# Performance work log

Measured on AMD Instinct MI355X. Metric: run time of the kernel, lower is better.

## Reference

```python
import jax, jax.numpy as jnp
import numpy as np


def _conv(x, w, b=None):
    # x: [B,C,H,W], w: [O,I,kh,kw], 'same' padding for odd kernels
    pad_h = (w.shape[2] - 1) // 2
    pad_w = (w.shape[3] - 1) // 2
    y = jax.lax.conv_general_dilated(
        x, w, window_strides=(1, 1),
        padding=[(pad_h, pad_h), (pad_w, pad_w)],
        dimension_numbers=("NCHW", "OIHW", "NCHW"))
    if b is not None:
        y = y + b[None, :, None, None]
    return y


def setup_inputs() -> dict:
    key = jax.random.key(0)
    ks = jax.random.split(key, 14)
    B, L_I, L_H, MAZE, F, OUT = 32, 8, 128, 64, 5, 16
    s = 0.05  # weight scale
    return {
        "X": jax.random.normal(ks[0], (B, L_I, MAZE, MAZE), jnp.float32),
        "hid_w": jax.random.normal(ks[1], (L_H, L_I, 3, 3), jnp.float32) * s,
        "hid_b": jax.random.normal(ks[2], (L_H,), jnp.float32) * s,
        "h0_w": jax.random.normal(ks[3], (L_H, L_H, 3, 3), jnp.float32) * s,
        "h0_b": jax.random.normal(ks[4], (L_H,), jnp.float32) * s,
        "c0_w": jax.random.normal(ks[5], (L_H, L_H, 3, 3), jnp.float32) * s,
        "c0_b": jax.random.normal(ks[6], (L_H,), jnp.float32) * s,
        "conv_w": jax.random.normal(ks[7], (1, L_H, F, F), jnp.float32) * s,
        "conv_b": jax.random.normal(ks[8], (1,), jnp.float32) * s,
        "W_ih": jax.random.normal(ks[9], (4 * L_H, 1), jnp.float32) * s,
        "W_hh": jax.random.normal(ks[10], (4 * L_H, L_H), jnp.float32) * s,
        "b_ih": jnp.zeros((4 * L_H,), jnp.float32),
        "b_hh": jnp.zeros((4 * L_H,), jnp.float32),
        "policy_w": jax.random.normal(ks[11], (OUT, L_H, 1, 1), jnp.float32) * s,
        "k": 10,
    }


def reference(X, hid_w, hid_b, h0_w, h0_b, c0_w, c0_b, conv_w, conv_b,
              W_ih, W_hh, b_ih, b_hh, policy_w, k):
    # hid: [B, l_h, H, W]
    hid = _conv(X, hid_w, hid_b)
    # torch .transpose(1,3).view(-1,l_h): keep as [B, W, H, l_h]
    h = jnp.transpose(_conv(hid, h0_w, h0_b), (0, 3, 2, 1))
    c = jnp.transpose(_conv(hid, c0_w, c0_b), (0, 3, 2, 1))
    bias = b_ih + b_hh

    def step(carry, _):
        h, c = carry
        h_map = jnp.transpose(h, (0, 3, 2, 1))          # [B, l_h, H, W]
        inp = jnp.transpose(_conv(h_map, conv_w, conv_b), (0, 3, 2, 1))  # [B,W,H,1]
        # PyTorch LSTMCell gate order: i, f, g, o
        gates = inp @ W_ih.T + h @ W_hh.T + bias        # [B, W, H, 4*l_h]
        i, f, g, o = jnp.split(gates, 4, axis=-1)
        c_new = jax.nn.sigmoid(f) * c + jax.nn.sigmoid(i) * jnp.tanh(g)
        h_new = jax.nn.sigmoid(o) * jnp.tanh(c_new)
        return (h_new, c_new), None

    (h, c), _ = jax.lax.scan(step, (h, c), None, length=k - 1)
    hk = jnp.transpose(h, (0, 3, 2, 1))                 # [B, l_h, H, W]
    logits = _conv(hk, policy_w, None)                  # 1x1 conv, no bias
    return logits
```

## Files before the change

kernel.cpp:

```cpp
#include <hip/hip_runtime.h>
#include <math.h>


typedef _Float16 f16;
typedef _Float16 f16x8 __attribute__((ext_vector_type(8)));
typedef float    f32x4 __attribute__((ext_vector_type(4)));

#define NB 32
#define HWD 64
#define NPIX (NB*HWD*HWD)

#define OB_HID   ((size_t)0)
#define OB_CC    ((size_t)33554432)
#define OB_HA    ((size_t)100663296)
#define OB_HB    ((size_t)134217728)
#define OB_DA    ((size_t)167772160)
#define OB_DB    ((size_t)176160768)
#define OB_WCB   ((size_t)184549376)
#define OB_WGB   ((size_t)185139200)
#define OB_WIB   ((size_t)185270272)
#define OB_W5B   ((size_t)185303040)
#define OB_BS2   ((size_t)185311232)
#define WS_BYTES ((size_t)185313280)

__device__ __forceinline__ float sigm(float x){ return 1.f/(1.f+__expf(-x)); }
__device__ __forceinline__ float tanhx(float x){ return 1.f - 2.f/(1.f+__expf(2.f*x)); }

__global__ void kTrans(const float* __restrict__ h0w, const float* __restrict__ c0w,
                       const float* __restrict__ whh, const float* __restrict__ cw5,
                       const float* __restrict__ wih, const float* __restrict__ bih,
                       const float* __restrict__ bhh, const float* __restrict__ cb,
                       f16* __restrict__ wcb, f16* __restrict__ wgb,
                       f16* __restrict__ wib, f16* __restrict__ w5b,
                       float* __restrict__ bs2)
{
    int e = blockIdx.x*256 + threadIdx.x;
    if (e < 294912) {
        int j = e & 7, l = (e >> 3) & 63, kk = (e >> 9) & 3;
        int nt = (e >> 11) & 15, tap = e >> 15;
        int c = (nt & 7)*16 + (l & 15);
        int k = kk*32 + (l >> 4)*8 + j;
        const float* src = (nt < 8) ? h0w : c0w;
        wcb[e] = (f16)src[((size_t)c*128 + k)*9 + tap];
    }
    if (e < 65536) {
        int j = e & 7, l = (e >> 3) & 63, fb = e >> 9;
        int nt = fb >> 2, kk = fb & 3;
        int cg = nt*16 + (l & 15), k = kk*32 + (l >> 4)*8 + j;
        wgb[e] = (f16)whh[(size_t)cg*128 + k];
    }
    if (e < 16384) {
        int l = (e >> 3) & 63, nt = e >> 9;
        wib[e] = (f16)wih[nt*16 + (l & 15)];
    }
    if (e < 4096) {
        int j = e & 7, l = (e >> 3) & 63, fb = e >> 9;
        int nt = fb >> 2, kk = fb & 3;
        int n = nt*16 + (l & 15), k = kk*32 + (l >> 4)*8 + j;
        w5b[e] = (n < 25) ? (f16)cw5[k*25 + n] : (f16)0.f;
    }
    if (e < 512) bs2[e] = bih[e] + bhh[e] + cb[0]*wih[e];
}

__global__ __launch_bounds__(256) void kHid(const float* __restrict__ X,
                                            const float* __restrict__ hw,
                                            const float* __restrict__ hb,
                                            f16* __restrict__ hid)
{
    __shared__ float Ws[128*73];
    __shared__ float Xs[6*6*8];
    int t = threadIdx.x;
    int blk = blockIdx.x;
    int b = blk >> 8, ti = (blk >> 4) & 15, tj = blk & 15;
    int i0 = ti*4, j0 = tj*4;
    for (int e = t; e < 9216; e += 256) {
        int c = e/72, q = e - c*72;
        Ws[c*73 + q] = hw[e];
    }
    for (int e = t; e < 288; e += 256) {
        int pos = e >> 3, ci = e & 7;
        int gi = i0 + pos/6 - 1, gj = j0 + pos%6 - 1;
        float v = 0.f;
        if ((unsigned)gi < 64u && (unsigned)gj < 64u)
            v = X[(((size_t)b*8 + ci)*64 + gi)*64 + gj];
        Xs[pos*8 + ci] = v;
    }
    __syncthreads();
    int c = t & 127, ph = t >> 7;
    float bv = hb[c];
    for (int p = ph*8; p < ph*8 + 8; ++p) {
        int pi = p >> 2, pj = p & 3;
        float acc = bv;
        #pragma unroll
        for (int ci = 0; ci < 8; ++ci)
            #pragma unroll
            for (int dy = 0; dy < 3; ++dy)
                #pragma unroll
                for (int dx = 0; dx < 3; ++dx)
                    acc += Xs[((pi+dy)*6 + (pj+dx))*8 + ci] * Ws[c*73 + ci*9 + dy*3 + dx];
        hid[(((size_t)b*64 + i0+pi)*64 + (j0+pj))*128 + c] = (f16)acc;
    }
}

__global__ __launch_bounds__(256,2) void kInit(const f16* __restrict__ hid,
                                               const f16* __restrict__ wcb,
                                               const f16* __restrict__ w5b,
                                               const float* __restrict__ h0b,
                                               const float* __restrict__ c0b,
                                               f16* __restrict__ h0out,
                                               float* __restrict__ cc,
                                               f16* __restrict__ dout)
{
    __shared__ f16 sHalo[100*128];
    int t = threadIdx.x;
    int blk = blockIdx.x;
    int b = blk >> 6, ti = (blk >> 3) & 7, tj = blk & 7;
    int i0 = ti*8, j0 = tj*8;
    int l = t & 63, wn = t >> 6;

    for (int e = t; e < 1600; e += 256) {
        int pos = e >> 4, ch = e & 15;
        int gi = i0 + pos/10 - 1, gj = j0 + pos%10 - 1;
        f16x8 v = {0,0,0,0,0,0,0,0};
        if ((unsigned)gi < 64u && (unsigned)gj < 64u)
            v = *(const f16x8*)(hid + ((((size_t)b*64 + gi)*64 + gj)*128) + ch*8);
        *(f16x8*)&sHalo[(pos*16 + (ch ^ (pos & 7)))*8] = v;
    }
    __syncthreads();

    f32x4 acc[4][4];
    #pragma unroll
    for (int mi = 0; mi < 4; ++mi)
        #pragma unroll
        for (int q = 0; q < 4; ++q) acc[mi][q] = (f32x4){0.f,0.f,0.f,0.f};

    for (int tap = 0; tap < 9; ++tap) {
        int dy = tap/3, dx = tap - dy*3;
        f16x8 a[4][4];
        #pragma unroll
        for (int mi = 0; mi < 4; ++mi) {
            int mrow = mi*16 + (l & 15);
            int pos = ((mrow >> 3) + dy)*10 + (mrow & 7) + dx;
            #pragma unroll
            for (int kk = 0; kk < 4; ++kk)
                a[mi][kk] = *(const f16x8*)&sHalo[(pos*16 + ((kk*4 + (l >> 4)) ^ (pos & 7)))*8];
        }
        #pragma unroll
        for (int q = 0; q < 4; ++q) {
            int nt = wn*4 + q;
            f16x8 bf[4];
            #pragma unroll
            for (int kk = 0; kk < 4; ++kk)
                bf[kk] = *(const f16x8*)(wcb + ((size_t)((tap*16 + nt)*4 + kk)*64 + l)*8);
            #pragma unroll
            for (int mi = 0; mi < 4; ++mi)
                #pragma unroll
                for (int kk = 0; kk < 4; ++kk)
                    acc[mi][q] = __builtin_amdgcn_mfma_f32_16x16x32_f16(a[mi][kk], bf[kk], acc[mi][q], 0, 0, 0);
        }
    }

    __syncthreads();
    f16* sH = sHalo;

    int cl = l & 15;
    bool isC = (wn >= 2);
    #pragma unroll
    for (int q = 0; q < 4; ++q) {
        int c = ((wn & 1)*4 + q)*16 + cl;
        float bv = isC ? c0b[c] : h0b[c];
        #pragma unroll
        for (int mi = 0; mi < 4; ++mi) {
            int mbase = mi*16 + (l >> 4)*4;
            if (isC) {
                float4 cv;
                cv.x = acc[mi][q][0] + bv; cv.y = acc[mi][q][1] + bv;
                cv.z = acc[mi][q][2] + bv; cv.w = acc[mi][q][3] + bv;
                *(float4*)(cc + (size_t)blk*8192 + (size_t)c*64 + mbase) = cv;
            } else {
                #pragma unroll
                for (int r = 0; r < 4; ++r) {
                    int m = mbase + r;
                    size_t gp = ((((size_t)b*64 + i0 + (m >> 3))*64 + j0 + (m & 7))*128) + c;
                    f16 hv = (f16)(acc[mi][q][r] + bv);
                    h0out[gp] = hv;
                    sH[(m*16 + ((c >> 3) ^ (m & 7)))*8 + (c & 7)] = hv;
                }
            }
        }
    }
    __syncthreads();

    {
        int m0 = wn*16 + (l & 15);
        f16x8 av[4];
        #pragma unroll
        for (int kk = 0; kk < 4; ++kk)
            av[kk] = *(const f16x8*)&sH[(m0*16 + ((kk*4 + (l >> 4)) ^ (m0 & 7)))*8];
        #pragma unroll
        for (int nt = 0; nt < 2; ++nt) {
            f32x4 dc = {0.f,0.f,0.f,0.f};
            #pragma unroll
            for (int kk = 0; kk < 4; ++kk)
                dc = __builtin_amdgcn_mfma_f32_16x16x32_f16(av[kk],
                        *(const f16x8*)(w5b + ((size_t)((nt*4 + kk)*64 + l))*8), dc, 0, 0, 0);
            #pragma unroll
            for (int r = 0; r < 4; ++r) {
                int mm = wn*16 + (l >> 4)*4 + r;
                size_t gp = ((((size_t)b*64 + i0 + (mm >> 3))*64 + j0 + (mm & 7))*32) + nt*16 + (l & 15);
                dout[gp] = (f16)dc[r];
            }
        }
    }
}

__global__ __launch_bounds__(256,4) void kFuse(const f16* __restrict__ hin,
                                               const f16* __restrict__ din,
                                               const f16* __restrict__ wgb,
                                               const f16* __restrict__ wib,
                                               const f16* __restrict__ w5b,
                                               const float* __restrict__ bs2,
                                               float* __restrict__ cc,
                                               f16* __restrict__ hout,
                                               f16* __restrict__ dout)
{
    __shared__ f16 sDH[144*32];
    __shared__ f16 sH[64*128];
    int t = threadIdx.x;
    int blk = blockIdx.x;
    int b = blk >> 6, ti = (blk >> 3) & 7, tj = blk & 7;
    int i0 = ti*8, j0 = tj*8;
    int l = t & 63, w = t >> 6;
    int wn = w >> 1, wm = w & 1;
    int cl = l & 15;

    f16x8 a[2][4];
    #pragma unroll
    for (int mi = 0; mi < 2; ++mi) {
        int m = (wm + mi*2)*16 + (l & 15);
        size_t gp = (((size_t)b*64 + i0 + (m >> 3))*64 + j0 + (m & 7))*128;
        #pragma unroll
        for (int kk = 0; kk < 4; ++kk)
            a[mi][kk] = *(const f16x8*)(hin + gp + kk*32 + (l >> 4)*8);
    }
    for (int e = t; e < 576; e += 256) {
        int pos = e >> 2, ch = e & 3;
        int gi = i0 + pos/12 - 2, gj = j0 + pos%12 - 2;
        f16x8 v = {0,0,0,0,0,0,0,0};
        if ((unsigned)gi < 64u && (unsigned)gj < 64u)
            v = *(const f16x8*)(din + (((size_t)b*64 + gi)*64 + gj)*32 + ch*8);
        *(f16x8*)&sDH[pos*32 + ch*8] = v;
    }
    __syncthreads();

    f16x8 adh[2];
    #pragma unroll
    for (int mi = 0; mi < 2; ++mi) {
        int m = (wm + mi*2)*16 + (l & 15);
        int pi = m >> 3, pj = m & 7;
        f16 tmp[8];
        #pragma unroll
        for (int j = 0; j < 8; ++j) {
            int kp = (l >> 4)*8 + j;
            int kpc = (kp < 25) ? kp : 0;
            int ty = kpc/5, tx = kpc - ty*5;
            f16 v = sDH[((pi + ty)*12 + (pj + tx))*32 + kpc];
            tmp[j] = (kp < 25) ? v : (f16)0.f;
        }
        adh[mi] = *(f16x8*)tmp;
    }

    bool doD = (dout != nullptr);
    #pragma unroll
    for (int q = 0; q < 4; ++q) {
        f32x4 acc2[2][4];
        #pragma unroll
        for (int mi = 0; mi < 2; ++mi)
            #pragma unroll
            for (int g = 0; g < 4; ++g) acc2[mi][g] = (f32x4){0.f,0.f,0.f,0.f};
        #pragma unroll
        for (int g = 0; g < 4; ++g) {
            int nt = g*8 + wn*4 + q;
            #pragma unroll
            for (int kk = 0; kk < 4; ++kk) {
                f16x8 bf = *(const f16x8*)(wgb + ((size_t)((nt*4 + kk)*64 + l))*8);
                #pragma unroll
                for (int mi = 0; mi < 2; ++mi)
                    acc2[mi][g] = __builtin_amdgcn_mfma_f32_16x16x32_f16(a[mi][kk], bf, acc2[mi][g], 0, 0, 0);
            }
            f16x8 be = *(const f16x8*)(wib + ((size_t)(nt*64 + l))*8);
            #pragma unroll
            for (int mi = 0; mi < 2; ++mi)
                acc2[mi][g] = __builtin_amdgcn_mfma_f32_16x16x32_f16(adh[mi], be, acc2[mi][g], 0, 0, 0);
        }
        int c = (wn*4 + q)*16 + cl;
        float bi = bs2[c], bff = bs2[128 + c], bg = bs2[256 + c], bo = bs2[384 + c];
        #pragma unroll
        for (int mi = 0; mi < 2; ++mi) {
            int mbase = (wm + mi*2)*16 + (l >> 4)*4;
            size_t cbase = (size_t)blk*8192 + (size_t)c*64 + mbase;
            float4 cold = *(const float4*)(cc + cbase);
            const float* cp = (const float*)&cold;
            float cn[4], hn[4];
            #pragma unroll
            for (int r = 0; r < 4; ++r) {
                float vi = acc2[mi][0][r] + bi;
                float vf = acc2[mi][1][r] + bff;
                float vg = acc2[mi][2][r] + bg;
                float vo = acc2[mi][3][r] + bo;
                float cv = sigm(vf)*cp[r] + sigm(vi)*tanhx(vg);
                cn[r] = cv;
                hn[r] = sigm(vo)*tanhx(cv);
            }
            *(float4*)(cc + cbase) = make_float4(cn[0], cn[1], cn[2], cn[3]);
            #pragma unroll
            for (int r = 0; r < 4; ++r) {
                int m = mbase + r;
                size_t gp = ((((size_t)b*64 + i0 + (m >> 3))*64 + j0 + (m & 7))*128) + c;
                f16 hv = (f16)hn[r];
                hout[gp] = hv;
                if (doD) sH[(m*16 + ((c >> 3) ^ (m & 7)))*8 + (c & 7)] = hv;
            }
        }
    }

    if (doD) {
        __syncthreads();
        int m0 = w*16 + (l & 15);
        f16x8 av[4];
        #pragma unroll
        for (int kk = 0; kk < 4; ++kk)
            av[kk] = *(const f16x8*)&sH[(m0*16 + ((kk*4 + (l >> 4)) ^ (m0 & 7)))*8];
        #pragma unroll
        for (int nt = 0; nt < 2; ++nt) {
            f32x4 dc = {0.f,0.f,0.f,0.f};
            #pragma unroll
            for (int kk = 0; kk < 4; ++kk)
                dc = __builtin_amdgcn_mfma_f32_16x16x32_f16(av[kk],
                        *(const f16x8*)(w5b + ((size_t)((nt*4 + kk)*64 + l))*8), dc, 0, 0, 0);
            #pragma unroll
            for (int r = 0; r < 4; ++r) {
                int mm = w*16 + (l >> 4)*4 + r;
                size_t gp = ((((size_t)b*64 + i0 + (mm >> 3))*64 + j0 + (mm & 7))*32) + nt*16 + (l & 15);
                dout[gp] = (f16)dc[r];
            }
        }
    }
}

__global__ __launch_bounds__(256) void kPolicy(const f16* __restrict__ h,
                                               const float* __restrict__ pw,
                                               float* __restrict__ out)
{
    __shared__ float Ps[16*128];
    int t = threadIdx.x;
    for (int e = t; e < 2048; e += 256) Ps[e] = pw[e];
    __syncthreads();
    size_t pid = (size_t)blockIdx.x*256 + t;
    int b = (int)(pid >> 12), rem = (int)(pid & 4095);
    float acc[16];
    #pragma unroll
    for (int o = 0; o < 16; ++o) acc[o] = 0.f;
    const f16x8* hb8 = (const f16x8*)(h + pid*128);
    #pragma unroll 2
    for (int k8 = 0; k8 < 16; ++k8) {
        f16x8 hv = hb8[k8];
        float hf[8];
        #pragma unroll
        for (int e = 0; e < 8; ++e) hf[e] = (float)hv[e];
        #pragma unroll
        for (int o = 0; o < 16; ++o) {
            float4 w0 = *(const float4*)&Ps[o*128 + k8*8];
            float4 w1 = *(const float4*)&Ps[o*128 + k8*8 + 4];
            acc[o] += hf[0]*w0.x + hf[1]*w0.y + hf[2]*w0.z + hf[3]*w0.w
                    + hf[4]*w1.x + hf[5]*w1.y + hf[6]*w1.z + hf[7]*w1.w;
        }
    }
    #pragma unroll
    for (int o = 0; o < 16; ++o)
        out[((size_t)b*16 + o)*4096 + rem] = acc[o];
}

extern "C" void kernel_launch(void* const* d_in, const int* in_sizes, int n_in,
                              void* d_out, int out_size, void* d_ws, size_t ws_size,
                              hipStream_t stream) {
    const float* X      = (const float*)d_in[0];
    const float* hid_w  = (const float*)d_in[1];
    const float* hid_b  = (const float*)d_in[2];
    const float* h0_w   = (const float*)d_in[3];
    const float* h0_b   = (const float*)d_in[4];
    const float* c0_w   = (const float*)d_in[5];
    const float* c0_b   = (const float*)d_in[6];
    const float* conv_w = (const float*)d_in[7];
    const float* conv_b = (const float*)d_in[8];
    const float* W_ih   = (const float*)d_in[9];
    const float* W_hh   = (const float*)d_in[10];
    const float* b_ih   = (const float*)d_in[11];
    const float* b_hh   = (const float*)d_in[12];
    const float* pol_w  = (const float*)d_in[13];

    if (ws_size < WS_BYTES) return;

    char* wsb = (char*)d_ws;
    f16*   HID = (f16*)  (wsb + OB_HID);
    float* CC  = (float*)(wsb + OB_CC);
    f16*   HA  = (f16*)  (wsb + OB_HA);
    f16*   HB  = (f16*)  (wsb + OB_HB);
    f16*   DA  = (f16*)  (wsb + OB_DA);
    f16*   DB  = (f16*)  (wsb + OB_DB);
    f16*   WCB = (f16*)  (wsb + OB_WCB);
    f16*   WGB = (f16*)  (wsb + OB_WGB);
    f16*   WIB = (f16*)  (wsb + OB_WIB);
    f16*   W5B = (f16*)  (wsb + OB_W5B);
    float* BS2 = (float*)(wsb + OB_BS2);

    kTrans<<<1152, 256, 0, stream>>>(h0_w, c0_w, W_hh, conv_w, W_ih, b_ih, b_hh, conv_b,
                                     WCB, WGB, WIB, W5B, BS2);
    kHid<<<8192, 256, 0, stream>>>(X, hid_w, hid_b, HID);
    kInit<<<2048, 256, 0, stream>>>(HID, WCB, W5B, h0_b, c0_b, HA, CC, DA);
    for (int st = 0; st < 9; ++st) {
        const f16* hin = (st & 1) ? HB : HA;
        const f16* din = (st & 1) ? DB : DA;
        f16* hout      = (st & 1) ? HA : HB;
        f16* dout      = (st & 1) ? DA : DB;
        if (st == 8) dout = nullptr;
        kFuse<<<2048, 256, 0, stream>>>(hin, din, WGB, WIB, W5B, BS2, CC, hout, dout);
    }
    kPolicy<<<512, 256, 0, stream>>>(HB, pol_w, (float*)d_out);
}
```

Baseline: 951.9 us.

## Fuse hidden conv into init kernel via MFMA and coalesce h stores through LDS

The separate fp32 kHid kernel is removed. The first 3x3 conv is now computed inside kInit with MFMA over a 10x10 halo tile recomputed from X, so the 32 MB hid intermediate is no longer written and read back. The h outputs of kInit and kFuse are now staged in shared memory and written as 16-byte vectorized stores instead of scattered 2-byte stores, and the cell-state loads in kFuse are issued early to overlap with other loads. In exchange the halo is recomputed per block, each block does more work, and kFuse gets an extra barrier and more registers.

```diff
diff --git a/kernel.cpp b/kernel.cpp
--- a/kernel.cpp
+++ b/kernel.cpp
@@ -10,29 +10,30 @@
 #define HWD 64
 #define NPIX (NB*HWD*HWD)
 
-#define OB_HID   ((size_t)0)
-#define OB_CC    ((size_t)33554432)
-#define OB_HA    ((size_t)100663296)
-#define OB_HB    ((size_t)134217728)
-#define OB_DA    ((size_t)167772160)
-#define OB_DB    ((size_t)176160768)
-#define OB_WCB   ((size_t)184549376)
-#define OB_WGB   ((size_t)185139200)
-#define OB_WIB   ((size_t)185270272)
-#define OB_W5B   ((size_t)185303040)
-#define OB_BS2   ((size_t)185311232)
-#define WS_BYTES ((size_t)185313280)
+#define OB_CC    ((size_t)0)
+#define OB_HA    ((size_t)67108864)
+#define OB_HB    ((size_t)100663296)
+#define OB_DA    ((size_t)134217728)
+#define OB_DB    ((size_t)142606336)
+#define OB_WCB   ((size_t)150994944)
+#define OB_WGB   ((size_t)151584768)
+#define OB_WIB   ((size_t)151715840)
+#define OB_W5B   ((size_t)151748608)
+#define OB_WHB   ((size_t)151756800)
+#define OB_BS2   ((size_t)151781376)
+#define WS_BYTES ((size_t)151783424)
 
 __device__ __forceinline__ float sigm(float x){ return 1.f/(1.f+__expf(-x)); }
 __device__ __forceinline__ float tanhx(float x){ return 1.f - 2.f/(1.f+__expf(2.f*x)); }
 
 __global__ void kTrans(const float* __restrict__ h0w, const float* __restrict__ c0w,
                        const float* __restrict__ whh, const float* __restrict__ cw5,
-                       const float* __restrict__ wih, const float* __restrict__ bih,
-                       const float* __restrict__ bhh, const float* __restrict__ cb,
+                       const float* __restrict__ wih, const float* __restrict__ hw,
+                       const float* __restrict__ bih, const float* __restrict__ bhh,
+                       const float* __restrict__ cb,
                        f16* __restrict__ wcb, f16* __restrict__ wgb,
                        f16* __restrict__ wib, f16* __restrict__ w5b,
-                       float* __restrict__ bs2)
+                       f16* __restrict__ whb, float* __restrict__ bs2)
 {
     int e = blockIdx.x*256 + threadIdx.x;
     if (e < 294912) {
@@ -53,6 +54,12 @@
         int l = (e >> 3) & 63, nt = e >> 9;
         wib[e] = (f16)wih[nt*16 + (l & 15)];
     }
+    if (e < 12288) {
+        int j = e & 7, l = (e >> 3) & 63, fb = e >> 9;
+        int nt = fb/3, kk = fb - nt*3;
+        int c = nt*16 + (l & 15), k = kk*32 + (l >> 4)*8 + j;
+        whb[e] = (k < 72) ? (f16)hw[(size_t)c*72 + (k & 7)*9 + (k >> 3)] : (f16)0.f;
+    }
     if (e < 4096) {
         int j = e & 7, l = (e >> 3) & 63, fb = e >> 9;
         int nt = fb >> 2, kk = fb & 3;
@@ -62,47 +69,9 @@
     if (e < 512) bs2[e] = bih[e] + bhh[e] + cb[0]*wih[e];
 }
 
-__global__ __launch_bounds__(256) void kHid(const float* __restrict__ X,
-                                            const float* __restrict__ hw,
-                                            const float* __restrict__ hb,
-                                            f16* __restrict__ hid)
-{
-    __shared__ float Ws[128*73];
-    __shared__ float Xs[6*6*8];
-    int t = threadIdx.x;
-    int blk = blockIdx.x;
-    int b = blk >> 8, ti = (blk >> 4) & 15, tj = blk & 15;
-    int i0 = ti*4, j0 = tj*4;
-    for (int e = t; e < 9216; e += 256) {
-        int c = e/72, q = e - c*72;
-        Ws[c*73 + q] = hw[e];
-    }
-    for (int e = t; e < 288; e += 256) {
-        int pos = e >> 3, ci = e & 7;
-        int gi = i0 + pos/6 - 1, gj = j0 + pos%6 - 1;
-        float v = 0.f;
-        if ((unsigned)gi < 64u && (unsigned)gj < 64u)
-            v = X[(((size_t)b*8 + ci)*64 + gi)*64 + gj];
-        Xs[pos*8 + ci] = v;
-    }
-    __syncthreads();
-    int c = t & 127, ph = t >> 7;
-    float bv = hb[c];
-    for (int p = ph*8; p < ph*8 + 8; ++p) {
-        int pi = p >> 2, pj = p & 3;
-        float acc = bv;
-        #pragma unroll
-        for (int ci = 0; ci < 8; ++ci)
-            #pragma unroll
-            for (int dy = 0; dy < 3; ++dy)
-                #pragma unroll
-                for (int dx = 0; dx < 3; ++dx)
-                    acc += Xs[((pi+dy)*6 + (pj+dx))*8 + ci] * Ws[c*73 + ci*9 + dy*3 + dx];
-        hid[(((size_t)b*64 + i0+pi)*64 + (j0+pj))*128 + c] = (f16)acc;
-    }
-}
-
-__global__ __launch_bounds__(256,2) void kInit(const f16* __restrict__ hid,
+__global__ __launch_bounds__(256,2) void kInit(const float* __restrict__ X,
+                                               const f16* __restrict__ whb,
+                                               const float* __restrict__ hidb,
                                                const f16* __restrict__ wcb,
                                                const f16* __restrict__ w5b,
                                                const float* __restrict__ h0b,
@@ -111,6 +80,7 @@
                                                float* __restrict__ cc,
                                                f16* __restrict__ dout)
 {
+    __shared__ f16 sX[1536];
     __shared__ f16 sHalo[100*128];
     int t = threadIdx.x;
     int blk = blockIdx.x;
@@ -118,13 +88,51 @@
     int i0 = ti*8, j0 = tj*8;
     int l = t & 63, wn = t >> 6;
 
-    for (int e = t; e < 1600; e += 256) {
-        int pos = e >> 4, ch = e & 15;
-        int gi = i0 + pos/10 - 1, gj = j0 + pos%10 - 1;
-        f16x8 v = {0,0,0,0,0,0,0,0};
-        if ((unsigned)gi < 64u && (unsigned)gj < 64u)
-            v = *(const f16x8*)(hid + ((((size_t)b*64 + gi)*64 + gj)*128) + ch*8);
-        *(f16x8*)&sHalo[(pos*16 + (ch ^ (pos & 7)))*8] = v;
+    for (int e = t; e < 1536; e += 256) {
+        if (e < 1152) {
+            int ci = e/144, pos = e - ci*144;
+            int gi = i0 + pos/12 - 2, gj = j0 + pos%12 - 2;
+            float xv = 0.f;
+            if ((unsigned)gi < 64u && (unsigned)gj < 64u)
+                xv = X[(((size_t)b*8 + ci)*64 + gi)*64 + gj];
+            sX[pos*8 + ci] = (f16)xv;
+        } else {
+            sX[e] = (f16)0.f;
+        }
+    }
+    __syncthreads();
+
+    for (int mt = wn; mt < 7; mt += 4) {
+        int m = mt*16 + (l & 15);
+        int pi = m/10, pj = m - pi*10;
+        f16x8 ax[3];
+        #pragma unroll
+        for (int kk = 0; kk < 3; ++kk) {
+            int tap = kk*4 + (l >> 4);
+            int dy = tap/3, dx = tap - dy*3;
+            ax[kk] = *(const f16x8*)&sX[((pi + dy)*12 + (pj + dx))*8];
+        }
+        #pragma unroll
+        for (int nt = 0; nt < 8; ++nt) {
+            f32x4 hc = {0.f,0.f,0.f,0.f};
+            #pragma unroll
+            for (int kk = 0; kk < 3; ++kk)
+                hc = __builtin_amdgcn_mfma_f32_16x16x32_f16(ax[kk],
+                        *(const f16x8*)(whb + ((size_t)(nt*3 + kk)*64 + l)*8), hc, 0, 0, 0);
+            int c = nt*16 + (l & 15);
+            float bv = hidb[c];
+            #pragma unroll
+            for (int r = 0; r < 4; ++r) {
+                int m2 = mt*16 + (l >> 4)*4 + r;
+                if (m2 < 100) {
+                    int pi2 = m2/10, pj2 = m2 - pi2*10;
+                    int gi = i0 + pi2 - 1, gj = j0 + pj2 - 1;
+                    bool inb = ((unsigned)gi < 64u && (unsigned)gj < 64u);
+                    sHalo[(m2*16 + ((c >> 3) ^ (m2 & 7)))*8 + (c & 7)] =
+                        inb ? (f16)(hc[r] + bv) : (f16)0.f;
+                }
+            }
+        }
     }
     __syncthreads();
 
@@ -181,10 +189,7 @@
                 #pragma unroll
                 for (int r = 0; r < 4; ++r) {
                     int m = mbase + r;
-                    size_t gp = ((((size_t)b*64 + i0 + (m >> 3))*64 + j0 + (m & 7))*128) + c;
-                    f16 hv = (f16)(acc[mi][q][r] + bv);
-                    h0out[gp] = hv;
-                    sH[(m*16 + ((c >> 3) ^ (m & 7)))*8 + (c & 7)] = hv;
+                    sH[(m*16 + ((c >> 3) ^ (m & 7)))*8 + (c & 7)] = (f16)(acc[mi][q][r] + bv);
                 }
             }
         }
@@ -211,6 +216,11 @@
                 dout[gp] = (f16)dc[r];
             }
         }
+    }
+    for (int e = t; e < 1024; e += 256) {
+        int pos = e >> 4, ch = e & 15;
+        f16x8 v = *(const f16x8*)&sH[(pos*16 + (ch ^ (pos & 7)))*8];
+        *(f16x8*)(h0out + ((((size_t)b*64 + i0 + (pos >> 3))*64 + j0 + (pos & 7))*128) + ch*8) = v;
     }
 }
 
@@ -243,6 +253,15 @@
         for (int kk = 0; kk < 4; ++kk)
             a[mi][kk] = *(const f16x8*)(hin + gp + kk*32 + (l >> 4)*8);
     }
+    float4 coldv[4][2];
+    #pragma unroll
+    for (int q = 0; q < 4; ++q)
+        #pragma unroll
+        for (int mi = 0; mi < 2; ++mi) {
+            int c = (wn*4 + q)*16 + cl;
+            int mbase = (wm + mi*2)*16 + (l >> 4)*4;
+            coldv[q][mi] = *(const float4*)(cc + (size_t)blk*8192 + (size_t)c*64 + mbase);
+        }
     for (int e = t; e < 576; e += 256) {
         int pos = e >> 2, ch = e & 3;
         int gi = i0 + pos/12 - 2, gj = j0 + pos%12 - 2;
@@ -299,8 +318,7 @@
         for (int mi = 0; mi < 2; ++mi) {
             int mbase = (wm + mi*2)*16 + (l >> 4)*4;
             size_t cbase = (size_t)blk*8192 + (size_t)c*64 + mbase;
-            float4 cold = *(const float4*)(cc + cbase);
-            const float* cp = (const float*)&cold;
+            const float* cp = (const float*)&coldv[q][mi];
             float cn[4], hn[4];
             #pragma unroll
             for (int r = 0; r < 4; ++r) {
@@ -316,16 +334,13 @@
             #pragma unroll
             for (int r = 0; r < 4; ++r) {
                 int m = mbase + r;
-                size_t gp = ((((size_t)b*64 + i0 + (m >> 3))*64 + j0 + (m & 7))*128) + c;
-                f16 hv = (f16)hn[r];
-                hout[gp] = hv;
-                if (doD) sH[(m*16 + ((c >> 3) ^ (m & 7)))*8 + (c & 7)] = hv;
-            }
-        }
-    }
-
+                sH[(m*16 + ((c >> 3) ^ (m & 7)))*8 + (c & 7)] = (f16)hn[r];
+            }
+        }
+    }
+
+    __syncthreads();
     if (doD) {
-        __syncthreads();
         int m0 = w*16 + (l & 15);
         f16x8 av[4];
         #pragma unroll
@@ -345,6 +360,11 @@
                 dout[gp] = (f16)dc[r];
             }
         }
+    }
+    for (int e = t; e < 1024; e += 256) {
+        int pos = e >> 4, ch = e & 15;
+        f16x8 v = *(const f16x8*)&sH[(pos*16 + (ch ^ (pos & 7)))*8];
+        *(f16x8*)(hout + ((((size_t)b*64 + i0 + (pos >> 3))*64 + j0 + (pos & 7))*128) + ch*8) = v;
     }
 }
 
@@ -402,7 +422,6 @@
     if (ws_size < WS_BYTES) return;
 
     char* wsb = (char*)d_ws;
-    f16*   HID = (f16*)  (wsb + OB_HID);
     float* CC  = (float*)(wsb + OB_CC);
     f16*   HA  = (f16*)  (wsb + OB_HA);
     f16*   HB  = (f16*)  (wsb + OB_HB);
@@ -412,12 +431,13 @@
     f16*   WGB = (f16*)  (wsb + OB_WGB);
     f16*   WIB = (f16*)  (wsb + OB_WIB);
     f16*   W5B = (f16*)  (wsb + OB_W5B);
+    f16*   WHB = (f16*)  (wsb + OB_WHB);
     float* BS2 = (float*)(wsb + OB_BS2);
 
-    kTrans<<<1152, 256, 0, stream>>>(h0_w, c0_w, W_hh, conv_w, W_ih, b_ih, b_hh, conv_b,
-                                     WCB, WGB, WIB, W5B, BS2);
-    kHid<<<8192, 256, 0, stream>>>(X, hid_w, hid_b, HID);
-    kInit<<<2048, 256, 0, stream>>>(HID, WCB, W5B, h0_b, c0_b, HA, CC, DA);
+    kTrans<<<1152, 256, 0, stream>>>(h0_w, c0_w, W_hh, conv_w, W_ih, hid_w,
+                                     b_ih, b_hh, conv_b,
+                                     WCB, WGB, WIB, W5B, WHB, BS2);
+    kInit<<<2048, 256, 0, stream>>>(X, WHB, hid_b, WCB, W5B, h0_b, c0_b, HA, CC, DA);
     for (int st = 0; st < 9; ++st) {
         const f16* hin = (st & 1) ? HB : HA;
         const f16* din = (st & 1) ? DB : DA;
```

Measured after the change: 900.6 us. -5.4%, faster.
